# Kernel optimization log

Measured on AMD Instinct MI355X. Metric: run time of the kernel, lower is better.

## Reference

```python
import jax, jax.numpy as jnp
import numpy as np

B, S, D, H, C = 8, 4096, 1024, 256, 512
INIT_RANGE = 0.01

def setup_inputs() -> dict:
    key = jax.random.key(0)
    ks = jax.random.split(key, 6)
    return {
        "hidden_states": jax.random.normal(ks[0], (B, S, D), dtype=jnp.float32),
        "conditions": jax.random.normal(ks[1], (B, C), dtype=jnp.float32),
        "down_project": jax.random.normal(ks[2], (D, H), dtype=jnp.float32) * INIT_RANGE,
        "down_gamma": jax.random.normal(ks[3], (C, H), dtype=jnp.float32),
        "down_beta": jnp.zeros((C, H), dtype=jnp.float32),
        "up_project": jax.random.normal(ks[4], (H, D), dtype=jnp.float32) * INIT_RANGE,
        "up_gamma": jax.random.normal(ks[5], (C, D), dtype=jnp.float32),
        "up_beta": jnp.zeros((C, D), dtype=jnp.float32),
    }

def reference(hidden_states, conditions, down_project, down_gamma, down_beta,
              up_project, up_gamma, up_beta):
    # per-example modulation coefficients: [B, H] / [B, D]
    dg = conditions @ down_gamma   # [B, H]
    db = conditions @ down_beta    # [B, H]
    ug = conditions @ up_gamma     # [B, D]
    ub = conditions @ up_beta      # [B, D]
    # per-example down weight: W_down * gamma (column scale) + beta (added to every row)
    w_down = down_project[None, :, :] * dg[:, None, :] + db[:, None, :]  # [B, D, H]
    down = jnp.einsum('bsd,bdh->bsh', hidden_states, w_down)             # [B, S, H]
    act = jax.nn.relu(down)
    w_up = up_project[None, :, :] * ug[:, None, :] + ub[:, None, :]      # [B, H, D]
    up = jnp.einsum('bsh,bhd->bsd', act, w_up)                           # [B, S, D]
    # (the original computes self.ln(up) but discards the result)
    return up + hidden_states
```

## Files before the change

### kernel.cpp

```cpp
#include <hip/hip_runtime.h>
#include <hip/hip_bf16.h>

typedef __attribute__((ext_vector_type(4))) float f32x4;
typedef __attribute__((ext_vector_type(8))) short s16x8;
typedef __attribute__((ext_vector_type(8))) unsigned short u16x8;
typedef __attribute__((ext_vector_type(4))) unsigned int u32x4;

#define DEVFN static __device__ __forceinline__

DEVFN unsigned short f2bf(float f) {
  union { float f; unsigned int u; } v; v.f = f;
  unsigned int u = v.u;
  u += 0x7fffu + ((u >> 16) & 1u);
  return (unsigned short)(u >> 16);
}

DEVFN unsigned int cvt_pk(float a, float b) {
  __hip_bfloat162 h = __float22bfloat162_rn(make_float2(a, b));
  union { __hip_bfloat162 h; unsigned int u; } v; v.h = h; return v.u;
}

DEVFN void gl_lds16(const void* g, void* l) {
  __builtin_amdgcn_global_load_lds((__attribute__((address_space(1))) void*)g,
                                   (__attribute__((address_space(3))) void*)l, 16, 0, 0);
}

#define DG_OFF 0
#define DB_OFF 2048
#define UG_OFF 4096
#define UB_OFF 12288
#define W1_BYTE 81920
#define W2_BYTE 606208

__global__ void prep_kernel(const float* __restrict__ cond,
                            const float* __restrict__ dgm, const float* __restrict__ dbt,
                            const float* __restrict__ ugm, const float* __restrict__ ubt,
                            const float* __restrict__ Wd, const float* __restrict__ Wu,
                            char* __restrict__ ws) {
  __shared__ float lc[4096];
  __shared__ float red[2048];
  const int t = threadIdx.x;

  if (blockIdx.x < 64) {
    const int bid = blockIdx.x;
    const float* src; char* dst; int C, ntile, kc;
    if (bid < 32) { src = Wd; C = 256;  ntile = bid >> 4; kc = bid & 15;
                    dst = ws + W1_BYTE + (size_t)(kc * 2 + ntile) * 16384; }
    else { int b2 = bid - 32; src = Wu; C = 1024; ntile = b2 >> 2; kc = b2 & 3;
           dst = ws + W2_BYTE + (size_t)(ntile * 4 + kc) * 16384; }
    const int n = t >> 1, kh = t & 1;
    const float* sp = src + (size_t)(kc * 64 + kh * 32) * C + ntile * 128 + n;
    unsigned short tmp[32];
#pragma unroll
    for (int kk = 0; kk < 32; ++kk) tmp[kk] = f2bf(sp[(size_t)kk * C]);
    char* drow = dst + n * 128;
#pragma unroll
    for (int gi = 0; gi < 4; ++gi) {
      u16x8 v;
#pragma unroll
      for (int e = 0; e < 8; ++e) v[e] = tmp[gi * 8 + e];
      int g = kh * 4 + gi;
      *(u16x8*)(drow + ((g ^ (n & 7)) << 4)) = v;
    }
    return;
  }

  float* coef = (float*)ws;
#pragma unroll
  for (int i = 0; i < 16; ++i) lc[t + i * 256] = cond[t + i * 256];
  __syncthreads();
  const int bid2 = blockIdx.x - 64;
  const int col = bid2 * 16 + (t & 15);
  const int ks = t >> 4;
  const float* src; int ncol, cl;
  if (col < 256)       { src = dgm; ncol = 256;  cl = col; }
  else if (col < 512)  { src = dbt; ncol = 256;  cl = col - 256; }
  else if (col < 1536) { src = ugm; ncol = 1024; cl = col - 512; }
  else                 { src = ubt; ncol = 1024; cl = col - 1536; }
  float acc[8] = {};
  for (int k = ks * 32; k < ks * 32 + 32; ++k) {
    float g = src[(size_t)k * ncol + cl];
#pragma unroll
    for (int b = 0; b < 8; ++b) acc[b] = fmaf(lc[b * 512 + k], g, acc[b]);
  }
#pragma unroll
  for (int b = 0; b < 8; ++b) red[(ks * 16 + (t & 15)) * 8 + b] = acc[b];
  __syncthreads();
  if (t < 128) {
    int c = t >> 3, b = t & 7;
    float s = 0.f;
#pragma unroll
    for (int k2 = 0; k2 < 16; ++k2) s += red[(k2 * 16 + c) * 8 + b];
    int colg = bid2 * 16 + c;
    float* dst; int ncol2, cl2;
    if (colg < 256)       { dst = coef + DG_OFF; ncol2 = 256;  cl2 = colg; }
    else if (colg < 512)  { dst = coef + DB_OFF; ncol2 = 256;  cl2 = colg - 256; }
    else if (colg < 1536) { dst = coef + UG_OFF; ncol2 = 1024; cl2 = colg - 512; }
    else                  { dst = coef + UB_OFF; ncol2 = 1024; cl2 = colg - 1536; }
    dst[b * ncol2 + cl2] = s;
  }
}

__global__ __launch_bounds__(512, 1)
void fused_kernel(const float* __restrict__ X, char* __restrict__ ws,
                  float* __restrict__ out) {
  __shared__ char lds[163840];
  const int tid = threadIdx.x;
  const int lane = tid & 63, wave = tid >> 6;
  const int lr = lane & 15, lq = lane >> 4;
  const int wm = wave >> 2, wn = wave & 3;

  const int m0 = blockIdx.x;
  const int row0 = m0 << 7;
  const int b = m0 >> 5;

  const float* coef = (const float*)ws;
  const char* w1 = ws + W1_BYTE;
  const char* w2 = ws + W2_BYTE;

  const int srow = tid >> 4, sg = tid & 15;
  const float* xsrc = X + (size_t)(row0 + srow) * 1024 + ((sg ^ (srow & 15)) << 2);

  int aoff[4][2][2], boff[4][2];
#pragma unroll
  for (int mf = 0; mf < 4; ++mf)
#pragma unroll
    for (int kf = 0; kf < 2; ++kf) {
      int r = wm * 64 + mf * 16 + lr;
      int g0 = kf * 8 + lq * 2;
      aoff[mf][kf][0] = r * 256 + ((g0 ^ (r & 15)) << 4);
      aoff[mf][kf][1] = r * 256 + (((g0 + 1) ^ (r & 15)) << 4);
    }
#pragma unroll
  for (int nf = 0; nf < 4; ++nf)
#pragma unroll
    for (int kf = 0; kf < 2; ++kf) {
      int n = wn * 64 + nf * 16 + lr;
      boff[nf][kf] = 131072 + (n >> 7) * 16384 + (n & 127) * 128 +
                     (((kf * 4 + lq) ^ (n & 7)) << 4);
    }

  f32x4 acc1[4][4] = {};
  float hacc[4] = {};

#define STAGE_X(t)                                                               \
  { char* xb = lds + 65536 + ((t) & 1) * 32768;                                  \
    _Pragma("unroll")                                                            \
    for (int i = 0; i < 4; ++i)                                                  \
      gl_lds16(xsrc + (size_t)((t) * 64) + (size_t)(i * 32) * 1024,              \
               xb + i * 8192 + tid * 16); }
#define STAGE_W1(t)                                                              \
  { _Pragma("unroll")                                                            \
    for (int i = 0; i < 4; ++i)                                                  \
      gl_lds16(w1 + (size_t)(t) * 32768 + i * 8192 + tid * 16,                   \
               lds + 131072 + i * 8192 + tid * 16); }

  STAGE_X(0); STAGE_X(1); STAGE_W1(0);
  asm volatile("s_waitcnt vmcnt(0)" ::: "memory");
  __builtin_amdgcn_sched_barrier(0);
  __builtin_amdgcn_s_barrier();
  __builtin_amdgcn_sched_barrier(0);

  for (int t = 0; t < 16; ++t) {
    const char* Xc = lds + 65536 + (t & 1) * 32768;
#pragma unroll
    for (int kf = 0; kf < 2; ++kf) {
      s16x8 afr[4], bfr[4];
#pragma unroll
      for (int mf = 0; mf < 4; ++mf) {
        f32x4 fa0 = *(const f32x4*)(Xc + aoff[mf][kf][0]);
        f32x4 fa1 = *(const f32x4*)(Xc + aoff[mf][kf][1]);
        if (wn == 0)
          hacc[mf] += fa0[0] + fa0[1] + fa0[2] + fa0[3] + fa1[0] + fa1[1] + fa1[2] + fa1[3];
        u32x4 p;
        p[0] = cvt_pk(fa0[0], fa0[1]); p[1] = cvt_pk(fa0[2], fa0[3]);
        p[2] = cvt_pk(fa1[0], fa1[1]); p[3] = cvt_pk(fa1[2], fa1[3]);
        union { u32x4 u; s16x8 s; } cv; cv.u = p; afr[mf] = cv.s;
      }
#pragma unroll
      for (int nf = 0; nf < 4; ++nf) bfr[nf] = *(const s16x8*)(lds + boff[nf][kf]);
#pragma unroll
      for (int mf = 0; mf < 4; ++mf)
#pragma unroll
        for (int nf = 0; nf < 4; ++nf)
          acc1[mf][nf] = __builtin_amdgcn_mfma_f32_16x16x32_bf16(afr[mf], bfr[nf], acc1[mf][nf], 0, 0, 0);
    }
    asm volatile("s_waitcnt lgkmcnt(0)" ::: "memory");
    __builtin_amdgcn_sched_barrier(0);
    __builtin_amdgcn_s_barrier();
    __builtin_amdgcn_sched_barrier(0);
    if (t < 15) {
      STAGE_W1(t + 1);
      if (t + 2 < 16) { STAGE_X(t + 2); asm volatile("s_waitcnt vmcnt(4)" ::: "memory"); }
      else            { asm volatile("s_waitcnt vmcnt(0)" ::: "memory"); }
      __builtin_amdgcn_sched_barrier(0);
      __builtin_amdgcn_s_barrier();
      __builtin_amdgcn_sched_barrier(0);
    }
  }

  float* hsumb = (float*)(lds + 65536);
  float* asp   = (float*)(lds + 65536 + 512);
  if (wn == 0) {
#pragma unroll
    for (int mf = 0; mf < 4; ++mf) {
      float s = hacc[mf];
      s += __shfl_xor(s, 16); s += __shfl_xor(s, 32);
      if (lq == 0) hsumb[wm * 64 + mf * 16 + lr] = s;
    }
  }
  __syncthreads();

  float dgv[4], dbv[4];
#pragma unroll
  for (int nf = 0; nf < 4; ++nf) {
    int h = wn * 64 + nf * 16 + lr;
    dgv[nf] = coef[DG_OFF + b * 256 + h];
    dbv[nf] = coef[DB_OFF + b * 256 + h];
  }

  float asacc[4][4] = {};
#pragma unroll
  for (int nf = 0; nf < 4; ++nf) {
    int g = nf * 2 + (lr >> 3);
    char* nbase = lds + wn * 16384 + (lr & 7) * 2;
    float dg_ = dgv[nf], db_ = dbv[nf];
#pragma unroll
    for (int mf = 0; mf < 4; ++mf) {
      int rb = wm * 64 + mf * 16 + lq * 4;
#pragma unroll
      for (int j = 0; j < 4; ++j) {
        int r = rb + j;
        float v = acc1[mf][nf][j] * dg_ + db_ * hsumb[r];
        v = fmaxf(v, 0.f);
        asacc[mf][j] += v;
        *(unsigned short*)(nbase + r * 128 + ((g ^ (r & 7)) << 4)) = f2bf(v);
      }
    }
  }
#pragma unroll
  for (int mf = 0; mf < 4; ++mf)
#pragma unroll
    for (int j = 0; j < 4; ++j) {
      float s = asacc[mf][j];
      s += __shfl_xor(s, 1); s += __shfl_xor(s, 2); s += __shfl_xor(s, 4); s += __shfl_xor(s, 8);
      if (lr == 0) asp[wn * 128 + wm * 64 + mf * 16 + lq * 4 + j] = s;
    }
  __syncthreads();

  float asv[4][4];
#pragma unroll
  for (int mf = 0; mf < 4; ++mf)
#pragma unroll
    for (int j = 0; j < 4; ++j) {
      int r = wm * 64 + mf * 16 + lq * 4 + j;
      asv[mf][j] = asp[r] + asp[128 + r] + asp[256 + r] + asp[384 + r];
    }
  float ugA[8][2], ubA[8][2];
#pragma unroll
  for (int nt = 0; nt < 8; ++nt)
#pragma unroll
    for (int nf = 0; nf < 2; ++nf) {
      int d = nt * 128 + wn * 32 + nf * 16 + lr;
      ugA[nt][nf] = coef[UG_OFF + b * 1024 + d];
      ubA[nt][nf] = coef[UB_OFF + b * 1024 + d];
    }

  int a2off[4][2], b2off[2][2];
#pragma unroll
  for (int mf = 0; mf < 4; ++mf)
#pragma unroll
    for (int kf = 0; kf < 2; ++kf) {
      int r = wm * 64 + mf * 16 + lr;
      a2off[mf][kf] = r * 128 + (((kf * 4 + lq) ^ (r & 7)) << 4);
    }
#pragma unroll
  for (int nf = 0; nf < 2; ++nf)
#pragma unroll
    for (int kf = 0; kf < 2; ++kf) {
      int nl = wn * 32 + nf * 16 + lr;
      b2off[nf][kf] = 131072 + nl * 128 + (((kf * 4 + lq) ^ (nl & 7)) << 4);
    }

#define STAGE_W2(s)                                                              \
  { _Pragma("unroll")                                                            \
    for (int i = 0; i < 2; ++i)                                                  \
      gl_lds16(w2 + (size_t)(s) * 16384 + i * 8192 + tid * 16,                   \
               lds + 131072 + ((s) & 1) * 16384 + i * 8192 + tid * 16); }

  STAGE_W2(0); STAGE_W2(1);
  asm volatile("s_waitcnt vmcnt(0)" ::: "memory");
  __builtin_amdgcn_sched_barrier(0);
  __builtin_amdgcn_s_barrier();
  __builtin_amdgcn_sched_barrier(0);

  f32x4 acc2[4][2];
  for (int s = 0; s < 32; ++s) {
    const int nt = s >> 2, kc = s & 3;
    if (kc == 0) {
#pragma unroll
      for (int mf = 0; mf < 4; ++mf)
#pragma unroll
        for (int nf = 0; nf < 2; ++nf) acc2[mf][nf] = (f32x4){0.f, 0.f, 0.f, 0.f};
    }
    const int bb = (s & 1) * 16384;
#pragma unroll
    for (int kf = 0; kf < 2; ++kf) {
      s16x8 afr[4], bfr[2];
#pragma unroll
      for (int mf = 0; mf < 4; ++mf)
        afr[mf] = *(const s16x8*)(lds + kc * 16384 + a2off[mf][kf]);
#pragma unroll
      for (int nf = 0; nf < 2; ++nf)
        bfr[nf] = *(const s16x8*)(lds + bb + b2off[nf][kf]);
#pragma unroll
      for (int mf = 0; mf < 4; ++mf)
#pragma unroll
        for (int nf = 0; nf < 2; ++nf)
          acc2[mf][nf] = __builtin_amdgcn_mfma_f32_16x16x32_bf16(afr[mf], bfr[nf], acc2[mf][nf], 0, 0, 0);
    }
    asm volatile("s_waitcnt lgkmcnt(0)" ::: "memory");
    __builtin_amdgcn_sched_barrier(0);
    __builtin_amdgcn_s_barrier();
    __builtin_amdgcn_sched_barrier(0);

    if (kc == 3) {
#pragma unroll
      for (int mf = 0; mf < 4; ++mf)
#pragma unroll
        for (int j = 0; j < 4; ++j) {
          int r = wm * 64 + mf * 16 + lq * 4 + j;
          size_t base = (size_t)(row0 + r) * 1024 + nt * 128;
          float as = asv[mf][j];
#pragma unroll
          for (int nf = 0; nf < 2; ++nf) {
            size_t gi = base + wn * 32 + nf * 16 + lr;
            out[gi] = acc2[mf][nf][j] * ugA[nt][nf] + ubA[nt][nf] * as + X[gi];
          }
        }
    }
    if (s + 2 < 32) STAGE_W2(s + 2);
    if (s < 31) {
      if (kc == 3 || s >= 30) asm volatile("s_waitcnt vmcnt(0)" ::: "memory");
      else                    asm volatile("s_waitcnt vmcnt(2)" ::: "memory");
      __builtin_amdgcn_sched_barrier(0);
      __builtin_amdgcn_s_barrier();
      __builtin_amdgcn_sched_barrier(0);
    }
  }
}

extern "C" void kernel_launch(void* const* d_in, const int* in_sizes, int n_in,
                              void* d_out, int out_size, void* d_ws, size_t ws_size,
                              hipStream_t stream) {
  const float* hidden       = (const float*)d_in[0];
  const float* conditions   = (const float*)d_in[1];
  const float* down_project = (const float*)d_in[2];
  const float* down_gamma   = (const float*)d_in[3];
  const float* down_beta    = (const float*)d_in[4];
  const float* up_project   = (const float*)d_in[5];
  const float* up_gamma     = (const float*)d_in[6];
  const float* up_beta      = (const float*)d_in[7];
  float* out = (float*)d_out;
  char* ws = (char*)d_ws;

  prep_kernel<<<224, 256, 0, stream>>>(conditions, down_gamma, down_beta, up_gamma, up_beta,
                                       down_project, up_project, ws);
  fused_kernel<<<256, 512, 0, stream>>>(hidden, ws, out);
}
```

Baseline: 96.72 us.

## Halve row tile to 64 rows, shrink LDS, and run more blocks per CU

```diff
diff --git a/kernel.cpp b/kernel.cpp
--- a/kernel.cpp
+++ b/kernel.cpp
@@ -4,7 +4,6 @@
 typedef __attribute__((ext_vector_type(4))) float f32x4;
 typedef __attribute__((ext_vector_type(8))) short s16x8;
 typedef __attribute__((ext_vector_type(8))) unsigned short u16x8;
-typedef __attribute__((ext_vector_type(4))) unsigned int u32x4;
 
 #define DEVFN static __device__ __forceinline__
 
@@ -41,26 +40,40 @@
   __shared__ float red[2048];
   const int t = threadIdx.x;
 
-  if (blockIdx.x < 64) {
-    const int bid = blockIdx.x;
-    const float* src; char* dst; int C, ntile, kc;
-    if (bid < 32) { src = Wd; C = 256;  ntile = bid >> 4; kc = bid & 15;
-                    dst = ws + W1_BYTE + (size_t)(kc * 2 + ntile) * 16384; }
-    else { int b2 = bid - 32; src = Wu; C = 1024; ntile = b2 >> 2; kc = b2 & 3;
-           dst = ws + W2_BYTE + (size_t)(ntile * 4 + kc) * 16384; }
-    const int n = t >> 1, kh = t & 1;
-    const float* sp = src + (size_t)(kc * 64 + kh * 32) * C + ntile * 128 + n;
+  if (blockIdx.x < 32) {
+    const int kc2 = blockIdx.x;
+    const int R = t >> 1, h = t & 1;
+    const float* sp = Wd + (size_t)(kc2 * 32) * 256 + 2 * R + h;
     unsigned short tmp[32];
 #pragma unroll
-    for (int kk = 0; kk < 32; ++kk) tmp[kk] = f2bf(sp[(size_t)kk * C]);
-    char* drow = dst + n * 128;
+    for (int kk = 0; kk < 32; ++kk) tmp[kk] = f2bf(sp[(size_t)kk * 256]);
+    char* dst = ws + W1_BYTE + (size_t)kc2 * 16384 + R * 128;
 #pragma unroll
     for (int gi = 0; gi < 4; ++gi) {
       u16x8 v;
 #pragma unroll
       for (int e = 0; e < 8; ++e) v[e] = tmp[gi * 8 + e];
+      int G = h * 4 + gi;
+      *(u16x8*)(dst + ((G ^ (R & 7)) << 4)) = v;
+    }
+    return;
+  }
+  if (blockIdx.x < 64) {
+    int b2 = blockIdx.x - 32;
+    int ntile = b2 >> 2, kc = b2 & 3;
+    const int n = t >> 1, kh = t & 1;
+    const float* sp = Wu + (size_t)(kc * 64 + kh * 32) * 1024 + ntile * 128 + n;
+    unsigned short tmp[32];
+#pragma unroll
+    for (int kk = 0; kk < 32; ++kk) tmp[kk] = f2bf(sp[(size_t)kk * 1024]);
+    char* dst = ws + W2_BYTE + (size_t)(ntile * 4 + kc) * 16384 + n * 128;
+#pragma unroll
+    for (int gi = 0; gi < 4; ++gi) {
+      u16x8 v;
+#pragma unroll
+      for (int e = 0; e < 8; ++e) v[e] = tmp[gi * 8 + e];
       int g = kh * 4 + gi;
-      *(u16x8*)(drow + ((g ^ (n & 7)) << 4)) = v;
+      *(u16x8*)(dst + ((g ^ (n & 7)) << 4)) = v;
     }
     return;
   }
@@ -101,140 +114,133 @@
   }
 }
 
-__global__ __launch_bounds__(512, 1)
+__global__ __launch_bounds__(512, 4)
 void fused_kernel(const float* __restrict__ X, char* __restrict__ ws,
                   float* __restrict__ out) {
-  __shared__ char lds[163840];
+  __shared__ char lds[81920];
   const int tid = threadIdx.x;
-  const int lane = tid & 63, wave = tid >> 6;
+  const int lane = tid & 63;
   const int lr = lane & 15, lq = lane >> 4;
-  const int wm = wave >> 2, wn = wave & 3;
-
-  const int m0 = blockIdx.x;
-  const int row0 = m0 << 7;
-  const int b = m0 >> 5;
+  const int wn = tid >> 6;
+
+  const int raw = blockIdx.x;
+  const int m = (raw & 7) * 64 + (raw >> 3);
+  const int row0 = m << 6;
+  const int b = m >> 6;
 
   const float* coef = (const float*)ws;
   const char* w1 = ws + W1_BYTE;
   const char* w2 = ws + W2_BYTE;
 
-  const int srow = tid >> 4, sg = tid & 15;
-  const float* xsrc = X + (size_t)(row0 + srow) * 1024 + ((sg ^ (srow & 15)) << 2);
-
-  int aoff[4][2][2], boff[4][2];
-#pragma unroll
-  for (int mf = 0; mf < 4; ++mf)
-#pragma unroll
-    for (int kf = 0; kf < 2; ++kf) {
-      int r = wm * 64 + mf * 16 + lr;
-      int g0 = kf * 8 + lq * 2;
-      aoff[mf][kf][0] = r * 256 + ((g0 ^ (r & 15)) << 4);
-      aoff[mf][kf][1] = r * 256 + (((g0 + 1) ^ (r & 15)) << 4);
-    }
-#pragma unroll
-  for (int nf = 0; nf < 4; ++nf)
-#pragma unroll
-    for (int kf = 0; kf < 2; ++kf) {
-      int n = wn * 64 + nf * 16 + lr;
-      boff[nf][kf] = 131072 + (n >> 7) * 16384 + (n & 127) * 128 +
-                     (((kf * 4 + lq) ^ (n & 7)) << 4);
-    }
-
-  f32x4 acc1[4][4] = {};
+  const int srow = tid >> 3, sg = tid & 7;
+  const float* xsrc = X + (size_t)(row0 + srow) * 1024 + ((sg ^ (srow & 7)) << 2);
+
+  int aoff[4][2], boff[2];
+#pragma unroll
+  for (int mf = 0; mf < 4; ++mf) {
+    int r = mf * 16 + lr;
+    aoff[mf][0] = r * 128 + (((2 * lq) ^ (r & 7)) << 4);
+    aoff[mf][1] = r * 128 + (((2 * lq + 1) ^ (r & 7)) << 4);
+  }
+#pragma unroll
+  for (int nf = 0; nf < 2; ++nf) {
+    int n = wn * 32 + nf * 16 + lr;
+    int R = n >> 1, G = (n & 1) * 4 + lq;
+    boff[nf] = R * 128 + ((G ^ (R & 7)) << 4);
+  }
+
+  f32x4 acc1[4][2] = {};
   float hacc[4] = {};
 
 #define STAGE_X(t)                                                               \
-  { char* xb = lds + 65536 + ((t) & 1) * 32768;                                  \
-    _Pragma("unroll")                                                            \
-    for (int i = 0; i < 4; ++i)                                                  \
-      gl_lds16(xsrc + (size_t)((t) * 64) + (size_t)(i * 32) * 1024,              \
-               xb + i * 8192 + tid * 16); }
+  gl_lds16(xsrc + (size_t)(t) * 32, lds + 32768 + ((t) & 1) * 8192 + tid * 16);
 #define STAGE_W1(t)                                                              \
   { _Pragma("unroll")                                                            \
-    for (int i = 0; i < 4; ++i)                                                  \
-      gl_lds16(w1 + (size_t)(t) * 32768 + i * 8192 + tid * 16,                   \
-               lds + 131072 + i * 8192 + tid * 16); }
-
-  STAGE_X(0); STAGE_X(1); STAGE_W1(0);
-  asm volatile("s_waitcnt vmcnt(0)" ::: "memory");
+    for (int i = 0; i < 2; ++i)                                                  \
+      gl_lds16(w1 + (size_t)(t) * 16384 + i * 8192 + tid * 16,                   \
+               lds + 49152 + ((t) & 1) * 16384 + i * 8192 + tid * 16); }
+
+  STAGE_X(0); STAGE_W1(0);
+  STAGE_X(1); STAGE_W1(1);
+  asm volatile("s_waitcnt vmcnt(3)" ::: "memory");
   __builtin_amdgcn_sched_barrier(0);
   __builtin_amdgcn_s_barrier();
   __builtin_amdgcn_sched_barrier(0);
 
-  for (int t = 0; t < 16; ++t) {
-    const char* Xc = lds + 65536 + (t & 1) * 32768;
-#pragma unroll
-    for (int kf = 0; kf < 2; ++kf) {
-      s16x8 afr[4], bfr[4];
-#pragma unroll
-      for (int mf = 0; mf < 4; ++mf) {
-        f32x4 fa0 = *(const f32x4*)(Xc + aoff[mf][kf][0]);
-        f32x4 fa1 = *(const f32x4*)(Xc + aoff[mf][kf][1]);
-        if (wn == 0)
-          hacc[mf] += fa0[0] + fa0[1] + fa0[2] + fa0[3] + fa1[0] + fa1[1] + fa1[2] + fa1[3];
-        u32x4 p;
-        p[0] = cvt_pk(fa0[0], fa0[1]); p[1] = cvt_pk(fa0[2], fa0[3]);
-        p[2] = cvt_pk(fa1[0], fa1[1]); p[3] = cvt_pk(fa1[2], fa1[3]);
-        union { u32x4 u; s16x8 s; } cv; cv.u = p; afr[mf] = cv.s;
-      }
-#pragma unroll
-      for (int nf = 0; nf < 4; ++nf) bfr[nf] = *(const s16x8*)(lds + boff[nf][kf]);
-#pragma unroll
-      for (int mf = 0; mf < 4; ++mf)
-#pragma unroll
-        for (int nf = 0; nf < 4; ++nf)
-          acc1[mf][nf] = __builtin_amdgcn_mfma_f32_16x16x32_bf16(afr[mf], bfr[nf], acc1[mf][nf], 0, 0, 0);
-    }
+  for (int t = 0; t < 32; ++t) {
+    const char* Xc = lds + 32768 + (t & 1) * 8192;
+    const char* Wc = lds + 49152 + (t & 1) * 16384;
+    s16x8 afr[4];
+#pragma unroll
+    for (int mf = 0; mf < 4; ++mf) {
+      f32x4 fa0 = *(const f32x4*)(Xc + aoff[mf][0]);
+      f32x4 fa1 = *(const f32x4*)(Xc + aoff[mf][1]);
+      if (wn == 0)
+        hacc[mf] += fa0[0] + fa0[1] + fa0[2] + fa0[3] + fa1[0] + fa1[1] + fa1[2] + fa1[3];
+      union { unsigned int u[4]; s16x8 s; } cv;
+      cv.u[0] = cvt_pk(fa0[0], fa0[1]); cv.u[1] = cvt_pk(fa0[2], fa0[3]);
+      cv.u[2] = cvt_pk(fa1[0], fa1[1]); cv.u[3] = cvt_pk(fa1[2], fa1[3]);
+      afr[mf] = cv.s;
+    }
+    s16x8 bfr[2];
+#pragma unroll
+    for (int nf = 0; nf < 2; ++nf) bfr[nf] = *(const s16x8*)(Wc + boff[nf]);
+#pragma unroll
+    for (int mf = 0; mf < 4; ++mf)
+#pragma unroll
+      for (int nf = 0; nf < 2; ++nf)
+        acc1[mf][nf] = __builtin_amdgcn_mfma_f32_16x16x32_bf16(afr[mf], bfr[nf], acc1[mf][nf], 0, 0, 0);
+
     asm volatile("s_waitcnt lgkmcnt(0)" ::: "memory");
     __builtin_amdgcn_sched_barrier(0);
     __builtin_amdgcn_s_barrier();
     __builtin_amdgcn_sched_barrier(0);
-    if (t < 15) {
-      STAGE_W1(t + 1);
-      if (t + 2 < 16) { STAGE_X(t + 2); asm volatile("s_waitcnt vmcnt(4)" ::: "memory"); }
-      else            { asm volatile("s_waitcnt vmcnt(0)" ::: "memory"); }
+    if (t + 2 < 32) { STAGE_X(t + 2); STAGE_W1(t + 2); }
+    if (t < 31) {
+      if (t + 2 < 32) asm volatile("s_waitcnt vmcnt(3)" ::: "memory");
+      else            asm volatile("s_waitcnt vmcnt(0)" ::: "memory");
       __builtin_amdgcn_sched_barrier(0);
       __builtin_amdgcn_s_barrier();
       __builtin_amdgcn_sched_barrier(0);
     }
   }
 
-  float* hsumb = (float*)(lds + 65536);
-  float* asp   = (float*)(lds + 65536 + 512);
-  if (wn == 0) {
-#pragma unroll
-    for (int mf = 0; mf < 4; ++mf) {
-      float s = hacc[mf];
-      s += __shfl_xor(s, 16); s += __shfl_xor(s, 32);
-      if (lq == 0) hsumb[wm * 64 + mf * 16 + lr] = s;
-    }
+  float* hsumb = (float*)(lds + 32768);
+  float* asp   = (float*)(lds + 33024);
+#pragma unroll
+  for (int mf = 0; mf < 4; ++mf) {
+    float s = hacc[mf];
+    s += __shfl_xor(s, 16); s += __shfl_xor(s, 32);
+    if (wn == 0 && lq == 0) hsumb[mf * 16 + lr] = s;
   }
   __syncthreads();
 
-  float dgv[4], dbv[4];
-#pragma unroll
-  for (int nf = 0; nf < 4; ++nf) {
-    int h = wn * 64 + nf * 16 + lr;
+  float dgv[2], dbv[2];
+#pragma unroll
+  for (int nf = 0; nf < 2; ++nf) {
+    int h = wn * 32 + nf * 16 + lr;
     dgv[nf] = coef[DG_OFF + b * 256 + h];
     dbv[nf] = coef[DB_OFF + b * 256 + h];
   }
 
   float asacc[4][4] = {};
-#pragma unroll
-  for (int nf = 0; nf < 4; ++nf) {
-    int g = nf * 2 + (lr >> 3);
-    char* nbase = lds + wn * 16384 + (lr & 7) * 2;
-    float dg_ = dgv[nf], db_ = dbv[nf];
-#pragma unroll
-    for (int mf = 0; mf < 4; ++mf) {
-      int rb = wm * 64 + mf * 16 + lq * 4;
-#pragma unroll
-      for (int j = 0; j < 4; ++j) {
-        int r = rb + j;
-        float v = acc1[mf][nf][j] * dg_ + db_ * hsumb[r];
-        v = fmaxf(v, 0.f);
-        asacc[mf][j] += v;
-        *(unsigned short*)(nbase + r * 128 + ((g ^ (r & 7)) << 4)) = f2bf(v);
+  {
+    char* kcb = lds + (wn >> 1) * 8192 + (lr & 7) * 2;
+#pragma unroll
+    for (int nf = 0; nf < 2; ++nf) {
+      int g = (wn & 1) * 4 + nf * 2 + (lr >> 3);
+      float dg_ = dgv[nf], db_ = dbv[nf];
+#pragma unroll
+      for (int mf = 0; mf < 4; ++mf) {
+        int rb = mf * 16 + lq * 4;
+#pragma unroll
+        for (int j = 0; j < 4; ++j) {
+          int r = rb + j;
+          float v = acc1[mf][nf][j] * dg_ + db_ * hsumb[r];
+          v = fmaxf(v, 0.f);
+          asacc[mf][j] += v;
+          *(unsigned short*)(kcb + r * 128 + ((g ^ (r & 7)) << 4)) = f2bf(v);
+        }
       }
     }
   }
@@ -244,7 +250,7 @@
     for (int j = 0; j < 4; ++j) {
       float s = asacc[mf][j];
       s += __shfl_xor(s, 1); s += __shfl_xor(s, 2); s += __shfl_xor(s, 4); s += __shfl_xor(s, 8);
-      if (lr == 0) asp[wn * 128 + wm * 64 + mf * 16 + lq * 4 + j] = s;
+      if (lr == 0) asp[wn * 64 + mf * 16 + lq * 4 + j] = s;
     }
   __syncthreads();
 
@@ -253,99 +259,89 @@
   for (int mf = 0; mf < 4; ++mf)
 #pragma unroll
     for (int j = 0; j < 4; ++j) {
-      int r = wm * 64 + mf * 16 + lq * 4 + j;
-      asv[mf][j] = asp[r] + asp[128 + r] + asp[256 + r] + asp[384 + r];
-    }
-  float ugA[8][2], ubA[8][2];
-#pragma unroll
-  for (int nt = 0; nt < 8; ++nt)
-#pragma unroll
-    for (int nf = 0; nf < 2; ++nf) {
-      int d = nt * 128 + wn * 32 + nf * 16 + lr;
-      ugA[nt][nf] = coef[UG_OFF + b * 1024 + d];
-      ubA[nt][nf] = coef[UB_OFF + b * 1024 + d];
-    }
-
-  int a2off[4][2], b2off[2][2];
+      int r = mf * 16 + lq * 4 + j;
+      float s = 0.f;
+#pragma unroll
+      for (int w = 0; w < 8; ++w) s += asp[w * 64 + r];
+      asv[mf][j] = s;
+    }
+  float ugA[8], ubA[8];
+#pragma unroll
+  for (int nt = 0; nt < 8; ++nt) {
+    int d = nt * 128 + wn * 16 + lr;
+    ugA[nt] = coef[UG_OFF + b * 1024 + d];
+    ubA[nt] = coef[UB_OFF + b * 1024 + d];
+  }
+
+  int a2off[4][2], b2off[2];
 #pragma unroll
   for (int mf = 0; mf < 4; ++mf)
 #pragma unroll
     for (int kf = 0; kf < 2; ++kf) {
-      int r = wm * 64 + mf * 16 + lr;
+      int r = mf * 16 + lr;
       a2off[mf][kf] = r * 128 + (((kf * 4 + lq) ^ (r & 7)) << 4);
     }
 #pragma unroll
-  for (int nf = 0; nf < 2; ++nf)
-#pragma unroll
-    for (int kf = 0; kf < 2; ++kf) {
-      int nl = wn * 32 + nf * 16 + lr;
-      b2off[nf][kf] = 131072 + nl * 128 + (((kf * 4 + lq) ^ (nl & 7)) << 4);
-    }
+  for (int kf = 0; kf < 2; ++kf) {
+    int nl = wn * 16 + lr;
+    b2off[kf] = nl * 128 + (((kf * 4 + lq) ^ (nl & 7)) << 4);
+  }
 
 #define STAGE_W2(s)                                                              \
   { _Pragma("unroll")                                                            \
     for (int i = 0; i < 2; ++i)                                                  \
       gl_lds16(w2 + (size_t)(s) * 16384 + i * 8192 + tid * 16,                   \
-               lds + 131072 + ((s) & 1) * 16384 + i * 8192 + tid * 16); }
-
+               lds + 49152 + ((s) & 1) * 16384 + i * 8192 + tid * 16); }
+
+  __builtin_amdgcn_sched_barrier(0);
   STAGE_W2(0); STAGE_W2(1);
-  asm volatile("s_waitcnt vmcnt(0)" ::: "memory");
+  asm volatile("s_waitcnt vmcnt(2)" ::: "memory");
   __builtin_amdgcn_sched_barrier(0);
   __builtin_amdgcn_s_barrier();
   __builtin_amdgcn_sched_barrier(0);
 
-  f32x4 acc2[4][2];
-  for (int s = 0; s < 32; ++s) {
-    const int nt = s >> 2, kc = s & 3;
-    if (kc == 0) {
-#pragma unroll
-      for (int mf = 0; mf < 4; ++mf)
-#pragma unroll
-        for (int nf = 0; nf < 2; ++nf) acc2[mf][nf] = (f32x4){0.f, 0.f, 0.f, 0.f};
-    }
-    const int bb = (s & 1) * 16384;
-#pragma unroll
-    for (int kf = 0; kf < 2; ++kf) {
-      s16x8 afr[4], bfr[2];
-#pragma unroll
-      for (int mf = 0; mf < 4; ++mf)
-        afr[mf] = *(const s16x8*)(lds + kc * 16384 + a2off[mf][kf]);
-#pragma unroll
-      for (int nf = 0; nf < 2; ++nf)
-        bfr[nf] = *(const s16x8*)(lds + bb + b2off[nf][kf]);
-#pragma unroll
-      for (int mf = 0; mf < 4; ++mf)
-#pragma unroll
-        for (int nf = 0; nf < 2; ++nf)
-          acc2[mf][nf] = __builtin_amdgcn_mfma_f32_16x16x32_bf16(afr[mf], bfr[nf], acc2[mf][nf], 0, 0, 0);
-    }
-    asm volatile("s_waitcnt lgkmcnt(0)" ::: "memory");
-    __builtin_amdgcn_sched_barrier(0);
-    __builtin_amdgcn_s_barrier();
-    __builtin_amdgcn_sched_barrier(0);
-
-    if (kc == 3) {
-#pragma unroll
-      for (int mf = 0; mf < 4; ++mf)
-#pragma unroll
-        for (int j = 0; j < 4; ++j) {
-          int r = wm * 64 + mf * 16 + lq * 4 + j;
-          size_t base = (size_t)(row0 + r) * 1024 + nt * 128;
-          float as = asv[mf][j];
-#pragma unroll
-          for (int nf = 0; nf < 2; ++nf) {
-            size_t gi = base + wn * 32 + nf * 16 + lr;
-            out[gi] = acc2[mf][nf][j] * ugA[nt][nf] + ubA[nt][nf] * as + X[gi];
-          }
-        }
-    }
-    if (s + 2 < 32) STAGE_W2(s + 2);
-    if (s < 31) {
-      if (kc == 3 || s >= 30) asm volatile("s_waitcnt vmcnt(0)" ::: "memory");
-      else                    asm volatile("s_waitcnt vmcnt(2)" ::: "memory");
+#pragma unroll
+  for (int nt = 0; nt < 8; ++nt) {
+    f32x4 acc2[4] = {};
+#pragma unroll
+    for (int kc = 0; kc < 4; ++kc) {
+      const int s = nt * 4 + kc;
+      const char* Ac = lds + kc * 8192;
+      const char* Wc2 = lds + 49152 + (kc & 1) * 16384;
+#pragma unroll
+      for (int kf = 0; kf < 2; ++kf) {
+        s16x8 a2[4], bb;
+#pragma unroll
+        for (int mf = 0; mf < 4; ++mf) a2[mf] = *(const s16x8*)(Ac + a2off[mf][kf]);
+        bb = *(const s16x8*)(Wc2 + b2off[kf]);
+#pragma unroll
+        for (int mf = 0; mf < 4; ++mf)
+          acc2[mf] = __builtin_amdgcn_mfma_f32_16x16x32_bf16(a2[mf], bb, acc2[mf], 0, 0, 0);
+      }
+      asm volatile("s_waitcnt lgkmcnt(0)" ::: "memory");
       __builtin_amdgcn_sched_barrier(0);
       __builtin_amdgcn_s_barrier();
       __builtin_amdgcn_sched_barrier(0);
+
+      if (s + 2 < 32) STAGE_W2(s + 2);
+      if (kc == 3) {
+#pragma unroll
+        for (int mf = 0; mf < 4; ++mf)
+#pragma unroll
+          for (int j = 0; j < 4; ++j) {
+            int r = mf * 16 + lq * 4 + j;
+            size_t gi = (size_t)(row0 + r) * 1024 + nt * 128 + wn * 16 + lr;
+            out[gi] = acc2[mf][j] * ugA[nt] + ubA[nt] * asv[mf][j] + X[gi];
+          }
+      }
+      if (s < 31) {
+        if (kc == 3)          asm volatile("s_waitcnt vmcnt(34)" ::: "memory");
+        else if (s + 2 < 32)  asm volatile("s_waitcnt vmcnt(2)"  ::: "memory");
+        else                  asm volatile("s_waitcnt vmcnt(0)"  ::: "memory");
+        __builtin_amdgcn_sched_barrier(0);
+        __builtin_amdgcn_s_barrier();
+        __builtin_amdgcn_sched_barrier(0);
+      }
     }
   }
 }
@@ -366,5 +362,5 @@
 
   prep_kernel<<<224, 256, 0, stream>>>(conditions, down_gamma, down_beta, up_gamma, up_beta,
                                        down_project, up_project, ws);
-  fused_kernel<<<256, 512, 0, stream>>>(hidden, ws, out);
-}
+  fused_kernel<<<512, 512, 0, stream>>>(hidden, ws, out);
+}
```

New measurement: 139.6 us. 1.44x slower.

## Deepen W2 staging to four buffers and prefetch residual X asynchronously

Applied to the files above, without the earlier changes.

```diff
diff --git a/kernel.cpp b/kernel.cpp
--- a/kernel.cpp
+++ b/kernel.cpp
@@ -24,6 +24,18 @@
   __builtin_amdgcn_global_load_lds((__attribute__((address_space(1))) void*)g,
                                    (__attribute__((address_space(3))) void*)l, 16, 0, 0);
 }
+
+DEVFN float async_ldf(const float* p) {
+  float v;
+  asm volatile("global_load_dword %0, %1, off"
+               : "=v"(v)
+               : "v"((unsigned long long)(uintptr_t)p)
+               : "memory");
+  return v;
+}
+
+#define SB() __builtin_amdgcn_sched_barrier(0)
+#define VMW(n) asm volatile("s_waitcnt vmcnt(" #n ")" ::: "memory")
 
 #define DG_OFF 0
 #define DB_OFF 2048
@@ -106,8 +118,8 @@
                   float* __restrict__ out) {
   __shared__ char lds[163840];
   const int tid = threadIdx.x;
-  const int lane = tid & 63, wave = tid >> 6;
-  const int lr = lane & 15, lq = lane >> 4;
+  const int lane = tid & 63, lr = lane & 15, lq = lane >> 4;
+  const int wave = tid >> 6;
   const int wm = wave >> 2, wn = wave & 3;
 
   const int m0 = blockIdx.x;
@@ -157,9 +169,7 @@
 
   STAGE_X(0); STAGE_X(1); STAGE_W1(0);
   asm volatile("s_waitcnt vmcnt(0)" ::: "memory");
-  __builtin_amdgcn_sched_barrier(0);
-  __builtin_amdgcn_s_barrier();
-  __builtin_amdgcn_sched_barrier(0);
+  SB(); __builtin_amdgcn_s_barrier(); SB();
 
   for (int t = 0; t < 16; ++t) {
     const char* Xc = lds + 65536 + (t & 1) * 32768;
@@ -186,16 +196,12 @@
           acc1[mf][nf] = __builtin_amdgcn_mfma_f32_16x16x32_bf16(afr[mf], bfr[nf], acc1[mf][nf], 0, 0, 0);
     }
     asm volatile("s_waitcnt lgkmcnt(0)" ::: "memory");
-    __builtin_amdgcn_sched_barrier(0);
-    __builtin_amdgcn_s_barrier();
-    __builtin_amdgcn_sched_barrier(0);
+    SB(); __builtin_amdgcn_s_barrier(); SB();
     if (t < 15) {
       STAGE_W1(t + 1);
       if (t + 2 < 16) { STAGE_X(t + 2); asm volatile("s_waitcnt vmcnt(4)" ::: "memory"); }
       else            { asm volatile("s_waitcnt vmcnt(0)" ::: "memory"); }
-      __builtin_amdgcn_sched_barrier(0);
-      __builtin_amdgcn_s_barrier();
-      __builtin_amdgcn_sched_barrier(0);
+      SB(); __builtin_amdgcn_s_barrier(); SB();
     }
   }
 
@@ -265,6 +271,7 @@
       ugA[nt][nf] = coef[UG_OFF + b * 1024 + d];
       ubA[nt][nf] = coef[UB_OFF + b * 1024 + d];
     }
+  __syncthreads();
 
   int a2off[4][2], b2off[2][2];
 #pragma unroll
@@ -279,73 +286,79 @@
 #pragma unroll
     for (int kf = 0; kf < 2; ++kf) {
       int nl = wn * 32 + nf * 16 + lr;
-      b2off[nf][kf] = 131072 + nl * 128 + (((kf * 4 + lq) ^ (nl & 7)) << 4);
+      b2off[nf][kf] = nl * 128 + (((kf * 4 + lq) ^ (nl & 7)) << 4);
     }
 
 #define STAGE_W2(s)                                                              \
   { _Pragma("unroll")                                                            \
     for (int i = 0; i < 2; ++i)                                                  \
       gl_lds16(w2 + (size_t)(s) * 16384 + i * 8192 + tid * 16,                   \
-               lds + 131072 + ((s) & 1) * 16384 + i * 8192 + tid * 16); }
-
-  STAGE_W2(0); STAGE_W2(1);
-  asm volatile("s_waitcnt vmcnt(0)" ::: "memory");
-  __builtin_amdgcn_sched_barrier(0);
-  __builtin_amdgcn_s_barrier();
-  __builtin_amdgcn_sched_barrier(0);
-
-  f32x4 acc2[4][2];
-  for (int s = 0; s < 32; ++s) {
-    const int nt = s >> 2, kc = s & 3;
-    if (kc == 0) {
-#pragma unroll
-      for (int mf = 0; mf < 4; ++mf)
-#pragma unroll
-        for (int nf = 0; nf < 2; ++nf) acc2[mf][nf] = (f32x4){0.f, 0.f, 0.f, 0.f};
-    }
-    const int bb = (s & 1) * 16384;
-#pragma unroll
-    for (int kf = 0; kf < 2; ++kf) {
-      s16x8 afr[4], bfr[2];
-#pragma unroll
-      for (int mf = 0; mf < 4; ++mf)
-        afr[mf] = *(const s16x8*)(lds + kc * 16384 + a2off[mf][kf]);
-#pragma unroll
-      for (int nf = 0; nf < 2; ++nf)
-        bfr[nf] = *(const s16x8*)(lds + bb + b2off[nf][kf]);
-#pragma unroll
-      for (int mf = 0; mf < 4; ++mf)
+               lds + 65536 + ((s) & 3) * 16384 + i * 8192 + tid * 16); }
+
+  STAGE_W2(0); STAGE_W2(1); STAGE_W2(2); STAGE_W2(3);
+  VMW(6);
+  SB(); __builtin_amdgcn_s_barrier(); SB();
+
+#pragma unroll
+  for (int nt = 0; nt < 8; ++nt) {
+    f32x4 acc2[4][2] = {};
+    float xres[4][4][2];
+#pragma unroll
+    for (int kc = 0; kc < 4; ++kc) {
+      const int s = nt * 4 + kc;
+      const char* Wb = lds + 65536 + (s & 3) * 16384;
+#pragma unroll
+      for (int kf = 0; kf < 2; ++kf) {
+        s16x8 a2[4], bb[2];
+#pragma unroll
+        for (int mf = 0; mf < 4; ++mf)
+          a2[mf] = *(const s16x8*)(lds + kc * 16384 + a2off[mf][kf]);
 #pragma unroll
         for (int nf = 0; nf < 2; ++nf)
-          acc2[mf][nf] = __builtin_amdgcn_mfma_f32_16x16x32_bf16(afr[mf], bfr[nf], acc2[mf][nf], 0, 0, 0);
-    }
-    asm volatile("s_waitcnt lgkmcnt(0)" ::: "memory");
-    __builtin_amdgcn_sched_barrier(0);
-    __builtin_amdgcn_s_barrier();
-    __builtin_amdgcn_sched_barrier(0);
-
-    if (kc == 3) {
-#pragma unroll
-      for (int mf = 0; mf < 4; ++mf)
-#pragma unroll
-        for (int j = 0; j < 4; ++j) {
-          int r = wm * 64 + mf * 16 + lq * 4 + j;
-          size_t base = (size_t)(row0 + r) * 1024 + nt * 128;
-          float as = asv[mf][j];
-#pragma unroll
-          for (int nf = 0; nf < 2; ++nf) {
-            size_t gi = base + wn * 32 + nf * 16 + lr;
-            out[gi] = acc2[mf][nf][j] * ugA[nt][nf] + ubA[nt][nf] * as + X[gi];
+          bb[nf] = *(const s16x8*)(Wb + b2off[nf][kf]);
+#pragma unroll
+        for (int mf = 0; mf < 4; ++mf)
+#pragma unroll
+          for (int nf = 0; nf < 2; ++nf)
+            acc2[mf][nf] = __builtin_amdgcn_mfma_f32_16x16x32_bf16(a2[mf], bb[nf], acc2[mf][nf], 0, 0, 0);
+      }
+      asm volatile("s_waitcnt lgkmcnt(0)" ::: "memory");
+      SB(); __builtin_amdgcn_s_barrier(); SB();
+
+      if (s + 4 < 32) STAGE_W2(s + 4);
+      if (kc == 0) {
+#pragma unroll
+        for (int mf = 0; mf < 4; ++mf)
+#pragma unroll
+          for (int j = 0; j < 4; ++j) {
+            int r = wm * 64 + mf * 16 + lq * 4 + j;
+            const float* gp = X + (size_t)(row0 + r) * 1024 + nt * 128 + wn * 32 + lr;
+            xres[mf][j][0] = async_ldf(gp);
+            xres[mf][j][1] = async_ldf(gp + 16);
           }
-        }
-    }
-    if (s + 2 < 32) STAGE_W2(s + 2);
-    if (s < 31) {
-      if (kc == 3 || s >= 30) asm volatile("s_waitcnt vmcnt(0)" ::: "memory");
-      else                    asm volatile("s_waitcnt vmcnt(2)" ::: "memory");
-      __builtin_amdgcn_sched_barrier(0);
-      __builtin_amdgcn_s_barrier();
-      __builtin_amdgcn_sched_barrier(0);
+      }
+
+      if (kc < 3) {
+        if (nt == 7)      { VMW(32); }
+        else if (kc == 0) { VMW(34); }
+        else              { VMW(38); }
+        SB(); __builtin_amdgcn_s_barrier(); SB();
+      } else {
+        if (nt == 7) { VMW(0); } else { VMW(6); }
+        SB();
+#pragma unroll
+        for (int mf = 0; mf < 4; ++mf)
+#pragma unroll
+          for (int j = 0; j < 4; ++j) {
+            int r = wm * 64 + mf * 16 + lq * 4 + j;
+            size_t gb = (size_t)(row0 + r) * 1024 + nt * 128 + wn * 32;
+#pragma unroll
+            for (int nf = 0; nf < 2; ++nf)
+              out[gb + nf * 16 + lr] =
+                  acc2[mf][nf][j] * ugA[nt][nf] + ubA[nt][nf] * asv[mf][j] + xres[mf][j][nf];
+          }
+        if (nt < 7) { SB(); __builtin_amdgcn_s_barrier(); SB(); }
+      }
     }
   }
 }
```

New measurement: 94.25 us. -2.6%, faster.
